# Performance work log

Measured on AMD Instinct MI355X. Metric: run time of the kernel, lower is better.

Reference implementation:

```python
import jax, jax.numpy as jnp
import numpy as np

B, T, K, H = 2, 2048, 1024, 16


def setup_inputs() -> dict:
    key = jax.random.key(0)
    ks = jax.random.split(key, 9)
    sc = 0.02
    return {
        "x": jax.random.normal(ks[0], (B, T, K), dtype=jnp.float32),
        "Wq_w": jax.random.normal(ks[1], (K, K), dtype=jnp.float32) * sc,
        "Wq_b": jax.random.normal(ks[2], (K,), dtype=jnp.float32) * sc,
        "Wk_w": jax.random.normal(ks[3], (K, K), dtype=jnp.float32) * sc,
        "Wk_b": jax.random.normal(ks[4], (K,), dtype=jnp.float32) * sc,
        "Wv_w": jax.random.normal(ks[5], (K, K), dtype=jnp.float32) * sc,
        "Wv_b": jax.random.normal(ks[6], (K,), dtype=jnp.float32) * sc,
        "Wo_w": jax.random.normal(ks[7], (K, K), dtype=jnp.float32) * sc,
        "Wo_b": jax.random.normal(ks[8], (K,), dtype=jnp.float32) * sc,
    }


def reference(x, Wq_w, Wq_b, Wk_w, Wk_b, Wv_w, Wv_b, Wo_w, Wo_b):
    b, t, k = x.shape
    h = H
    s = k // h
    # nn.Linear: y = x @ W^T + b
    q = x @ Wq_w.T + Wq_b
    kk = x @ Wk_w.T + Wk_b
    v = x @ Wv_w.T + Wv_b
    # [b, t, h, s] -> [b, h, t, s]
    q = q.reshape(b, t, h, s).transpose(0, 2, 1, 3)
    kk = kk.reshape(b, t, h, s).transpose(0, 2, 1, 3)
    v = v.reshape(b, t, h, s).transpose(0, 2, 1, 3)
    # scores [b, h, t, t]
    dot = jnp.einsum("bhqd,bhkd->bhqk", q, kk)
    # causal mask: upper triangle (offset=1) set to -inf BEFORE scaling
    causal = jnp.tril(jnp.ones((t, t), dtype=bool))
    dot = jnp.where(causal, dot, -jnp.inf)
    # NOTE: original scales by sqrt(k) (full model dim), not sqrt(head_dim)
    dot = dot / jnp.sqrt(jnp.asarray(k, dot.dtype))
    attn = jax.nn.softmax(dot, axis=-1)
    out = jnp.einsum("bhqk,bhkd->bhqd", attn, v)  # [b, h, t, s]
    out = out.transpose(0, 2, 1, 3).reshape(b, t, k)
    return out @ Wo_w.T + Wo_b
```

## Files before the change

### kernel.cpp

```cpp
#include <hip/hip_runtime.h>

typedef unsigned short u16;
typedef unsigned int u32;
typedef __bf16 bf16x8 __attribute__((ext_vector_type(8)));
typedef float f32x4 __attribute__((ext_vector_type(4)));
typedef unsigned short u16x8 __attribute__((ext_vector_type(8)));
typedef unsigned int u32x4 __attribute__((ext_vector_type(4)));

#define B_ 2
#define T_ 2048
#define K_ 1024
#define H_ 16
#define S_ 64
#define MKC 4194304
#define QSCALE 0.04508422f

__device__ __forceinline__ u16 f2bf(float f) {
  unsigned int u = __builtin_bit_cast(unsigned int, f);
  u += 0x7fffu + ((u >> 16) & 1u);
  return (u16)(u >> 16);
}

__device__ __forceinline__ f32x4 MFMA(bf16x8 a, bf16x8 b, f32x4 c) {
  return __builtin_amdgcn_mfma_f32_16x16x32_bf16(a, b, c, 0, 0, 0);
}

__device__ __forceinline__ void gld16(const void* g, void* l) {
  __builtin_amdgcn_global_load_lds((const __attribute__((address_space(1))) void*)g,
                                   (__attribute__((address_space(3))) void*)l, 16, 0, 0);
}

template <int N>
__device__ __forceinline__ void waitv() {
  asm volatile("s_waitcnt vmcnt(%0)" ::"i"(N) : "memory");
}
__device__ __forceinline__ void memfence_barrier() {
  asm volatile("" ::: "memory");
  __builtin_amdgcn_s_barrier();
}
__device__ __forceinline__ float fmax3(float a, float b, float c) {
  return fmaxf(fmaxf(a, b), c);
}

__global__ __launch_bounds__(256) void cvt_all(const float* __restrict__ x,
                                               const float* __restrict__ W0,
                                               const float* __restrict__ W1,
                                               const float* __restrict__ W2,
                                               const float* __restrict__ W3,
                                               u16* __restrict__ xb,
                                               u16* __restrict__ wb) {
  const int i = blockIdx.x * 256 + threadIdx.x;
  const float* src;
  u16* dst;
  if (i < 524288) {
    src = x + (size_t)i * 8;
    dst = xb + (size_t)i * 8;
  } else {
    const int j = i - 524288;
    const int sel = j >> 17;
    const float* W = sel == 0 ? W0 : sel == 1 ? W1 : sel == 2 ? W2 : W3;
    src = W + (size_t)(j & 131071) * 8;
    dst = wb + (size_t)j * 8;
  }
  const float4* s = (const float4*)src;
  float4 f0 = s[0], f1 = s[1];
  u16x8 p;
  p[0] = f2bf(f0.x); p[1] = f2bf(f0.y); p[2] = f2bf(f0.z); p[3] = f2bf(f0.w);
  p[4] = f2bf(f1.x); p[5] = f2bf(f1.y); p[6] = f2bf(f1.z); p[7] = f2bf(f1.w);
  *(u16x8*)dst = p;
}

template <int OMODE, int BN>
__global__ __launch_bounds__(256) void gemm16(const u16* __restrict__ A,
                                              const u16* __restrict__ Bm,
                                              const float* __restrict__ b0,
                                              const float* __restrict__ b1,
                                              const float* __restrict__ b2,
                                              void* __restrict__ C0,
                                              int M, int N, int K) {
  constexpr int NF = BN / 32;
  constexpr int SOPS = 2 + BN / 64;
  __shared__ u16 As[2][128 * 32];
  __shared__ u16 Bs[2][BN * 32];
  const int bm = blockIdx.x * 128;
  const int bn = blockIdx.y * BN;
  const int tid = threadIdx.x;
  const int w = tid >> 6, lane = tid & 63;
  const int wr = (w >> 1) * 64, wc = (w & 1) * (BN / 2);
  const int lr = lane & 15, g = lane >> 4;
  const int lk = g * 8;
  const int srow = lane >> 2, scol = (lane & 3) * 8;

  f32x4 acc[4][NF] = {};

  auto stg = [&](int buf, int k0) {
#pragma unroll
    for (int i = 0; i < 2; ++i) {
      const int rbase = (i * 4 + w) * 16;
      gld16(A + (size_t)(bm + rbase + srow) * K + k0 + scol, &As[buf][rbase * 32]);
    }
#pragma unroll
    for (int i = 0; i < BN / 64; ++i) {
      const int rbase = (i * 4 + w) * 16;
      gld16(Bm + (size_t)(bn + rbase + srow) * K + k0 + scol, &Bs[buf][rbase * 32]);
    }
  };

  stg(0, 0);
  const int NK = K >> 5;
  for (int kk = 0; kk < NK; ++kk) {
    const int buf = kk & 1;
    const bool pf = (kk + 1 < NK);
    if (pf) {
      stg(buf ^ 1, (kk + 1) * 32);
      waitv<SOPS>();
    } else {
      waitv<0>();
    }
    __builtin_amdgcn_s_barrier();
    bf16x8 af[4], bfr[NF];
#pragma unroll
    for (int m = 0; m < 4; ++m)
      af[m] = *(const bf16x8*)&As[buf][(wr + m * 16 + lr) * 32 + lk];
#pragma unroll
    for (int n = 0; n < NF; ++n)
      bfr[n] = *(const bf16x8*)&Bs[buf][(wc + n * 16 + lr) * 32 + lk];
#pragma unroll
    for (int m = 0; m < 4; ++m)
#pragma unroll
      for (int n = 0; n < NF; ++n)
        acc[m][n] = MFMA(af[m], bfr[n], acc[m][n]);
    memfence_barrier();
  }

  const int sel = (OMODE == 2) ? 0 : (bn >> 10);
  const float* bp = (OMODE == 2) ? b0 : (sel == 0 ? b0 : sel == 1 ? b1 : b2);
#pragma unroll
  for (int n = 0; n < NF; ++n) {
    const int col = bn + wc + n * 16 + lr;
    const float bv = bp[(OMODE == 2) ? col : (col & 1023)];
#pragma unroll
    for (int m = 0; m < 4; ++m) {
#pragma unroll
      for (int r = 0; r < 4; ++r) {
        const int row = bm + wr + m * 16 + g * 4 + r;
        float v = acc[m][n][r] + bv;
        if (OMODE == 2) {
          ((float*)C0)[(size_t)row * N + col] = v;
        } else {
          u16* dst = (u16*)C0;
          const int cc = col & 1023;
          if (sel == 2) {
            const int bb = row >> 11, t = row & 2047, hh = cc >> 6, ss = cc & 63;
            dst[(size_t)2 * MKC + (((size_t)(bb * H_ + hh) * S_ + ss) << 11) + t] = f2bf(v);
          } else {
            if (sel == 0) v *= QSCALE;
            dst[(size_t)sel * MKC + (size_t)row * 1024 + cc] = f2bf(v);
          }
        }
      }
    }
  }
}

__global__ __launch_bounds__(256) void attn_fwd(const u16* __restrict__ Q,
                                                const u16* __restrict__ Kb,
                                                const u16* __restrict__ Vt,
                                                u16* __restrict__ O) {
  __shared__ u16 Ks[2][64 * 64];
  __shared__ u16 Vs[2][64 * 64];
  const int tid = threadIdx.x;
  const int w = tid >> 6, lane = tid & 63;
  const int qh = lane & 15;
  const int g = lane >> 4;
  const int bh = blockIdx.x;
  const int b = bh >> 4, h = bh & 15;
  const int yy = blockIdx.y, t7 = yy & 7, kq = yy >> 3;
  const int qtile = (kq == 0) ? (31 - t7) : (kq == 1) ? (16 + t7)
                   : (kq == 2) ? (15 - t7) : t7;
  const int qb = qtile * 64;
  const int qw = qb + w * 16;
  const int myq = qw + qh;

  const size_t qoff = (size_t)(b * T_ + qw + qh) * K_ + h * S_ + g * 8;
  const bf16x8 bq0 = *(const bf16x8*)(Q + qoff);
  const bf16x8 bq1 = *(const bf16x8*)(Q + qoff + 32);

  const int srow = lane >> 3;
  const int sl8 = ((lane & 7) ^ srow) * 8;
  int kvp[2];
#pragma unroll
  for (int i = 0; i < 2; ++i) {
    const int rho = w * 16 + i * 8 + srow;
    const int a = rho >> 4;
    kvp[i] = ((a >> 1) << 5) | (((rho >> 2) & 3) << 3) | ((a & 1) << 2) | (rho & 3);
  }
  const u16* kq0 = Kb + (size_t)(b * T_ + kvp[0]) * K_ + h * S_ + sl8;
  const u16* kq1 = Kb + (size_t)(b * T_ + kvp[1]) * K_ + h * S_ + sl8;
  const u16* vq0 = Vt + (size_t)(bh * S_ + w * 16 + srow) * T_ + sl8;
  const u16* vq1 = Vt + (size_t)(bh * S_ + w * 16 + 8 + srow) * T_ + sl8;
  auto stage = [&](int buf) {
    gld16(kq0, &Ks[buf][(w * 16) * 64]);
    gld16(kq1, &Ks[buf][(w * 16 + 8) * 64]);
    gld16(vq0, &Vs[buf][(w * 16) * 64]);
    gld16(vq1, &Vs[buf][(w * 16 + 8) * 64]);
    kq0 += 64 * K_; kq1 += 64 * K_; vq0 += 64; vq1 += 64;
  };

  const int nk = qtile + 1;
  stage(0);

  float m = -INFINITY;
  f32x4 o[4] = {};
  f32x4 o_l = {};
  const int ksw = qh & 7;
  u16x8 ov;
#pragma unroll
  for (int i = 0; i < 8; ++i) ov[i] = 0x3F80;
  const bf16x8 ones = __builtin_bit_cast(bf16x8, ov);

  for (int kt = 0; kt < nk; ++kt) {
    const int k0 = kt * 64;
    const int cur = kt & 1;
    const bool pf = (kt + 1 < nk);
    if (pf) {
      stage(cur ^ 1);
      waitv<4>();
    } else {
      waitv<0>();
    }
    __builtin_amdgcn_s_barrier();

    f32x4 s[4];
    __builtin_amdgcn_s_setprio(1);
#pragma unroll
    for (int a = 0; a < 4; ++a) {
      const u16* kr = &Ks[cur][(a * 16 + qh) * 64];
      const bf16x8 kf0 = *(const bf16x8*)(kr + ((g ^ ksw) * 8));
      const bf16x8 kf1 = *(const bf16x8*)(kr + (((4 + g) ^ ksw) * 8));
      f32x4 z = {0.f, 0.f, 0.f, 0.f};
      z = MFMA(kf0, bq0, z);
      s[a] = MFMA(kf1, bq1, z);
    }
    __builtin_amdgcn_s_setprio(0);

    float p[4][4];
    if (k0 + 63 > qw) {
      const int thr = myq - k0 - (g << 3);
#pragma unroll
      for (int a = 0; a < 4; ++a)
#pragma unroll
        for (int r = 0; r < 4; ++r) {
          const int C = ((a >> 1) << 5) + ((a & 1) << 2) + r;
          p[a][r] = (C <= thr) ? s[a][r] : -INFINITY;
        }
    } else {
#pragma unroll
      for (int a = 0; a < 4; ++a)
#pragma unroll
        for (int r = 0; r < 4; ++r) p[a][r] = s[a][r];
    }
    float x0 = fmax3(p[0][0], p[0][1], p[0][2]);
    float x1 = fmax3(p[0][3], p[1][0], p[1][1]);
    float x2 = fmax3(p[1][2], p[1][3], p[2][0]);
    float x3 = fmax3(p[2][1], p[2][2], p[2][3]);
    float x4 = fmax3(p[3][0], p[3][1], p[3][2]);
    float vmax = fmax3(fmax3(x0, x1, x2), x3, fmaxf(x4, p[3][3]));
    vmax = fmaxf(vmax, __shfl_xor(vmax, 16));
    vmax = fmaxf(vmax, __shfl_xor(vmax, 32));

    if (__any(vmax > m + 11.5f)) {
      const float mnew = fmaxf(m, vmax);
      const float alpha = __builtin_amdgcn_exp2f(m - mnew);
      m = mnew;
      float aR[4];
#pragma unroll
      for (int r = 0; r < 4; ++r) aR[r] = __shfl(alpha, 4 * g + r);
#pragma unroll
      for (int nn = 0; nn < 4; ++nn)
#pragma unroll
        for (int r = 0; r < 4; ++r) o[nn][r] *= aR[r];
#pragma unroll
      for (int r = 0; r < 4; ++r) o_l[r] *= aR[r];
    }

#pragma unroll
    for (int a = 0; a < 4; ++a)
#pragma unroll
      for (int r = 0; r < 4; ++r)
        p[a][r] = __builtin_amdgcn_exp2f(p[a][r] - m);

    __builtin_amdgcn_s_setprio(1);
#pragma unroll
    for (int c = 0; c < 2; ++c) {
      u32 t0, t1, t2, t3;
      asm("v_cvt_pk_bf16_f32 %0, %1, %2" : "=v"(t0) : "v"(p[2 * c][0]), "v"(p[2 * c][1]));
      asm("v_cvt_pk_bf16_f32 %0, %1, %2" : "=v"(t1) : "v"(p[2 * c][2]), "v"(p[2 * c][3]));
      asm("v_cvt_pk_bf16_f32 %0, %1, %2" : "=v"(t2) : "v"(p[2 * c + 1][0]), "v"(p[2 * c + 1][1]));
      asm("v_cvt_pk_bf16_f32 %0, %1, %2" : "=v"(t3) : "v"(p[2 * c + 1][2]), "v"(p[2 * c + 1][3]));
      u32x4 tv; tv[0] = t0; tv[1] = t1; tv[2] = t2; tv[3] = t3;
      const bf16x8 pa = __builtin_bit_cast(bf16x8, tv);
      o_l = MFMA(pa, ones, o_l);
#pragma unroll
      for (int nn = 0; nn < 4; ++nn) {
        const bf16x8 vf =
            *(const bf16x8*)(&Vs[cur][(16 * nn + qh) * 64] + (((c * 4 + g) ^ ksw) * 8));
        o[nn] = MFMA(pa, vf, o[nn]);
      }
    }
    __builtin_amdgcn_s_setprio(0);

    memfence_barrier();
  }

#pragma unroll
  for (int r = 0; r < 4; ++r) {
    const float inv = 1.f / o_l[r];
    const size_t row = (size_t)(b * T_ + qw + 4 * g + r);
#pragma unroll
    for (int nn = 0; nn < 4; ++nn)
      O[row * K_ + h * S_ + nn * 16 + qh] = f2bf(o[nn][r] * inv);
  }
}

extern "C" void kernel_launch(void* const* d_in, const int* in_sizes, int n_in,
                              void* d_out, int out_size, void* d_ws, size_t ws_size,
                              hipStream_t stream) {
  (void)in_sizes; (void)n_in; (void)out_size; (void)ws_size;
  const float* x  = (const float*)d_in[0];
  const float* Wq = (const float*)d_in[1];
  const float* bq = (const float*)d_in[2];
  const float* Wk = (const float*)d_in[3];
  const float* bk = (const float*)d_in[4];
  const float* Wv = (const float*)d_in[5];
  const float* bv = (const float*)d_in[6];
  const float* Wo = (const float*)d_in[7];
  const float* bo = (const float*)d_in[8];
  float* out = (float*)d_out;

  const size_t MK = (size_t)MKC;
  const size_t WK = (size_t)K_ * K_;
  u16* Qb  = (u16*)d_ws;
  u16* Kbf = Qb + MK;
  u16* Vtb = Kbf + MK;
  u16* AO  = Vtb + MK;
  u16* xb  = AO + MK;
  u16* Wqkv = xb + MK;
  u16* Wob  = Wqkv + 3 * WK;

  dim3 blk(256);
  cvt_all<<<dim3(4096), blk, 0, stream>>>(x, Wq, Wk, Wv, Wo, xb, Wqkv);
  gemm16<3, 128><<<dim3(32, 24), blk, 0, stream>>>(xb, Wqkv, bq, bk, bv, Qb,
                                                   B_ * T_, 3 * K_, K_);
  attn_fwd<<<dim3(B_ * H_, T_ / 64), blk, 0, stream>>>(Qb, Kbf, Vtb, AO);
  gemm16<2, 64><<<dim3(32, 16), blk, 0, stream>>>(AO, Wob, bo, bo, bo, out,
                                                  B_ * T_, K_, K_);
}
```

Before: 109.7 us.

## Pair causal q-tiles per block and software-pipeline QK^T with softmax-PV

Each attention block now handles two query tiles (yy and 31-yy) in sequence, which balances causal work across blocks and halves the grid. Inside each tile the loop is restructured so the QK^T MFMAs for the next KV tile are issued before the softmax and PV of the current one, with K and V prefetches split and ordered separately. This aims to overlap the matrix-core work with the exp/max work and to even out per-block runtime, at the cost of fewer resident blocks, more live registers, and a serial second segment per block.

```diff
diff --git a/kernel.cpp b/kernel.cpp
--- a/kernel.cpp
+++ b/kernel.cpp
@@ -175,16 +175,7 @@
   const int g = lane >> 4;
   const int bh = blockIdx.x;
   const int b = bh >> 4, h = bh & 15;
-  const int yy = blockIdx.y, t7 = yy & 7, kq = yy >> 3;
-  const int qtile = (kq == 0) ? (31 - t7) : (kq == 1) ? (16 + t7)
-                   : (kq == 2) ? (15 - t7) : t7;
-  const int qb = qtile * 64;
-  const int qw = qb + w * 16;
-  const int myq = qw + qh;
-
-  const size_t qoff = (size_t)(b * T_ + qw + qh) * K_ + h * S_ + g * 8;
-  const bf16x8 bq0 = *(const bf16x8*)(Q + qoff);
-  const bf16x8 bq1 = *(const bf16x8*)(Q + qoff + 32);
+  const int yy = blockIdx.y;
 
   const int srow = lane >> 3;
   const int sl8 = ((lane & 7) ^ srow) * 8;
@@ -195,131 +186,166 @@
     const int a = rho >> 4;
     kvp[i] = ((a >> 1) << 5) | (((rho >> 2) & 3) << 3) | ((a & 1) << 2) | (rho & 3);
   }
-  const u16* kq0 = Kb + (size_t)(b * T_ + kvp[0]) * K_ + h * S_ + sl8;
-  const u16* kq1 = Kb + (size_t)(b * T_ + kvp[1]) * K_ + h * S_ + sl8;
-  const u16* vq0 = Vt + (size_t)(bh * S_ + w * 16 + srow) * T_ + sl8;
-  const u16* vq1 = Vt + (size_t)(bh * S_ + w * 16 + 8 + srow) * T_ + sl8;
-  auto stage = [&](int buf) {
-    gld16(kq0, &Ks[buf][(w * 16) * 64]);
-    gld16(kq1, &Ks[buf][(w * 16 + 8) * 64]);
-    gld16(vq0, &Vs[buf][(w * 16) * 64]);
-    gld16(vq1, &Vs[buf][(w * 16 + 8) * 64]);
-    kq0 += 64 * K_; kq1 += 64 * K_; vq0 += 64; vq1 += 64;
-  };
-
-  const int nk = qtile + 1;
-  stage(0);
-
-  float m = -INFINITY;
-  f32x4 o[4] = {};
-  f32x4 o_l = {};
   const int ksw = qh & 7;
   u16x8 ov;
 #pragma unroll
   for (int i = 0; i < 8; ++i) ov[i] = 0x3F80;
   const bf16x8 ones = __builtin_bit_cast(bf16x8, ov);
 
-  for (int kt = 0; kt < nk; ++kt) {
-    const int k0 = kt * 64;
-    const int cur = kt & 1;
-    const bool pf = (kt + 1 < nk);
-    if (pf) {
-      stage(cur ^ 1);
-      waitv<4>();
-    } else {
-      waitv<0>();
-    }
+  for (int seg = 0; seg < 2; ++seg) {
+    const int qtile = seg ? (31 - yy) : yy;
+    const int qb = qtile * 64;
+    const int qw = qb + w * 16;
+    const int myq = qw + qh;
+    const int nk = qtile + 1;
+
+    const size_t qoff = (size_t)(b * T_ + qw + qh) * K_ + h * S_ + g * 8;
+    const bf16x8 bq0 = *(const bf16x8*)(Q + qoff);
+    const bf16x8 bq1 = *(const bf16x8*)(Q + qoff + 32);
+
+    const u16* kq0 = Kb + (size_t)(b * T_ + kvp[0]) * K_ + h * S_ + sl8;
+    const u16* kq1 = Kb + (size_t)(b * T_ + kvp[1]) * K_ + h * S_ + sl8;
+    const u16* vq0 = Vt + (size_t)(bh * S_ + w * 16 + srow) * T_ + sl8;
+    const u16* vq1 = Vt + (size_t)(bh * S_ + w * 16 + 8 + srow) * T_ + sl8;
+
+    auto stageK = [&](int buf) {
+      gld16(kq0, &Ks[buf][(w * 16) * 64]);
+      gld16(kq1, &Ks[buf][(w * 16 + 8) * 64]);
+      kq0 += 64 * K_; kq1 += 64 * K_;
+    };
+    auto stageV = [&](int buf) {
+      gld16(vq0, &Vs[buf][(w * 16) * 64]);
+      gld16(vq1, &Vs[buf][(w * 16 + 8) * 64]);
+      vq0 += 64; vq1 += 64;
+    };
+
+    float m = -INFINITY;
+    f32x4 o[4] = {};
+    f32x4 o_l = {};
+    f32x4 sA[4], sB[4];
+
+    auto QKT = [&](int buf, f32x4 (&sO)[4]) {
+      __builtin_amdgcn_s_setprio(1);
+#pragma unroll
+      for (int a = 0; a < 4; ++a) {
+        const u16* kr = &Ks[buf][(a * 16 + qh) * 64];
+        const bf16x8 kf0 = *(const bf16x8*)(kr + ((g ^ ksw) * 8));
+        const bf16x8 kf1 = *(const bf16x8*)(kr + (((4 + g) ^ ksw) * 8));
+        f32x4 z = {0.f, 0.f, 0.f, 0.f};
+        z = MFMA(kf0, bq0, z);
+        sO[a] = MFMA(kf1, bq1, z);
+      }
+      __builtin_amdgcn_s_setprio(0);
+    };
+
+    auto SMPV = [&](f32x4 (&sIn)[4], int buf, int k0) {
+      float p[4][4];
+      if (k0 + 63 > qw) {
+        const int thr = myq - k0 - (g << 3);
+#pragma unroll
+        for (int a = 0; a < 4; ++a)
+#pragma unroll
+          for (int r = 0; r < 4; ++r) {
+            const int C = ((a >> 1) << 5) + ((a & 1) << 2) + r;
+            p[a][r] = (C <= thr) ? sIn[a][r] : -INFINITY;
+          }
+      } else {
+#pragma unroll
+        for (int a = 0; a < 4; ++a)
+#pragma unroll
+          for (int r = 0; r < 4; ++r) p[a][r] = sIn[a][r];
+      }
+      float x0 = fmax3(p[0][0], p[0][1], p[0][2]);
+      float x1 = fmax3(p[0][3], p[1][0], p[1][1]);
+      float x2 = fmax3(p[1][2], p[1][3], p[2][0]);
+      float x3 = fmax3(p[2][1], p[2][2], p[2][3]);
+      float x4 = fmax3(p[3][0], p[3][1], p[3][2]);
+      float vmax = fmax3(fmax3(x0, x1, x2), x3, fmaxf(x4, p[3][3]));
+      vmax = fmaxf(vmax, __shfl_xor(vmax, 16));
+      vmax = fmaxf(vmax, __shfl_xor(vmax, 32));
+
+      if (__any(vmax > m + 11.5f)) {
+        const float mnew = fmaxf(m, vmax);
+        const float alpha = __builtin_amdgcn_exp2f(m - mnew);
+        m = mnew;
+        float aR[4];
+#pragma unroll
+        for (int r = 0; r < 4; ++r) aR[r] = __shfl(alpha, 4 * g + r);
+#pragma unroll
+        for (int nn = 0; nn < 4; ++nn)
+#pragma unroll
+          for (int r = 0; r < 4; ++r) o[nn][r] *= aR[r];
+#pragma unroll
+        for (int r = 0; r < 4; ++r) o_l[r] *= aR[r];
+      }
+
+#pragma unroll
+      for (int a = 0; a < 4; ++a)
+#pragma unroll
+        for (int r = 0; r < 4; ++r)
+          p[a][r] = __builtin_amdgcn_exp2f(p[a][r] - m);
+
+      __builtin_amdgcn_s_setprio(1);
+#pragma unroll
+      for (int c = 0; c < 2; ++c) {
+        u32 t0, t1, t2, t3;
+        asm("v_cvt_pk_bf16_f32 %0, %1, %2" : "=v"(t0) : "v"(p[2 * c][0]), "v"(p[2 * c][1]));
+        asm("v_cvt_pk_bf16_f32 %0, %1, %2" : "=v"(t1) : "v"(p[2 * c][2]), "v"(p[2 * c][3]));
+        asm("v_cvt_pk_bf16_f32 %0, %1, %2" : "=v"(t2) : "v"(p[2 * c + 1][0]), "v"(p[2 * c + 1][1]));
+        asm("v_cvt_pk_bf16_f32 %0, %1, %2" : "=v"(t3) : "v"(p[2 * c + 1][2]), "v"(p[2 * c + 1][3]));
+        u32x4 tv; tv[0] = t0; tv[1] = t1; tv[2] = t2; tv[3] = t3;
+        const bf16x8 pa = __builtin_bit_cast(bf16x8, tv);
+        o_l = MFMA(pa, ones, o_l);
+#pragma unroll
+        for (int nn = 0; nn < 4; ++nn) {
+          const bf16x8 vf =
+              *(const bf16x8*)(&Vs[buf][(16 * nn + qh) * 64] + (((c * 4 + g) ^ ksw) * 8));
+          o[nn] = MFMA(pa, vf, o[nn]);
+        }
+      }
+      __builtin_amdgcn_s_setprio(0);
+    };
+
+    stageK(0); stageV(0);
+    waitv<0>();
     __builtin_amdgcn_s_barrier();
-
-    f32x4 s[4];
-    __builtin_amdgcn_s_setprio(1);
-#pragma unroll
-    for (int a = 0; a < 4; ++a) {
-      const u16* kr = &Ks[cur][(a * 16 + qh) * 64];
-      const bf16x8 kf0 = *(const bf16x8*)(kr + ((g ^ ksw) * 8));
-      const bf16x8 kf1 = *(const bf16x8*)(kr + (((4 + g) ^ ksw) * 8));
-      f32x4 z = {0.f, 0.f, 0.f, 0.f};
-      z = MFMA(kf0, bq0, z);
-      s[a] = MFMA(kf1, bq1, z);
-    }
-    __builtin_amdgcn_s_setprio(0);
-
-    float p[4][4];
-    if (k0 + 63 > qw) {
-      const int thr = myq - k0 - (g << 3);
-#pragma unroll
-      for (int a = 0; a < 4; ++a)
-#pragma unroll
-        for (int r = 0; r < 4; ++r) {
-          const int C = ((a >> 1) << 5) + ((a & 1) << 2) + r;
-          p[a][r] = (C <= thr) ? s[a][r] : -INFINITY;
-        }
-    } else {
-#pragma unroll
-      for (int a = 0; a < 4; ++a)
-#pragma unroll
-        for (int r = 0; r < 4; ++r) p[a][r] = s[a][r];
-    }
-    float x0 = fmax3(p[0][0], p[0][1], p[0][2]);
-    float x1 = fmax3(p[0][3], p[1][0], p[1][1]);
-    float x2 = fmax3(p[1][2], p[1][3], p[2][0]);
-    float x3 = fmax3(p[2][1], p[2][2], p[2][3]);
-    float x4 = fmax3(p[3][0], p[3][1], p[3][2]);
-    float vmax = fmax3(fmax3(x0, x1, x2), x3, fmaxf(x4, p[3][3]));
-    vmax = fmaxf(vmax, __shfl_xor(vmax, 16));
-    vmax = fmaxf(vmax, __shfl_xor(vmax, 32));
-
-    if (__any(vmax > m + 11.5f)) {
-      const float mnew = fmaxf(m, vmax);
-      const float alpha = __builtin_amdgcn_exp2f(m - mnew);
-      m = mnew;
-      float aR[4];
-#pragma unroll
-      for (int r = 0; r < 4; ++r) aR[r] = __shfl(alpha, 4 * g + r);
+    QKT(0, sA);
+    if (nk > 1) { stageK(1); stageV(1); }
+
+    int kt = 0;
+    for (;;) {
+      {
+        const bool hn = kt + 1 < nk;
+        if (hn) waitv<2>(); else waitv<0>();
+        __builtin_amdgcn_s_barrier();
+        if (hn) { QKT(1, sB); if (kt + 2 < nk) stageK(0); }
+        SMPV(sA, 0, kt * 64);
+        memfence_barrier();
+        if (kt + 2 < nk) stageV(0);
+        if (!hn) break;
+        ++kt;
+      }
+      {
+        const bool hn = kt + 1 < nk;
+        if (hn) waitv<2>(); else waitv<0>();
+        __builtin_amdgcn_s_barrier();
+        if (hn) { QKT(0, sA); if (kt + 2 < nk) stageK(1); }
+        SMPV(sB, 1, kt * 64);
+        memfence_barrier();
+        if (kt + 2 < nk) stageV(1);
+        if (!hn) break;
+        ++kt;
+      }
+    }
+
+#pragma unroll
+    for (int r = 0; r < 4; ++r) {
+      const float inv = 1.f / o_l[r];
+      const size_t row = (size_t)(b * T_ + qw + 4 * g + r);
 #pragma unroll
       for (int nn = 0; nn < 4; ++nn)
-#pragma unroll
-        for (int r = 0; r < 4; ++r) o[nn][r] *= aR[r];
-#pragma unroll
-      for (int r = 0; r < 4; ++r) o_l[r] *= aR[r];
-    }
-
-#pragma unroll
-    for (int a = 0; a < 4; ++a)
-#pragma unroll
-      for (int r = 0; r < 4; ++r)
-        p[a][r] = __builtin_amdgcn_exp2f(p[a][r] - m);
-
-    __builtin_amdgcn_s_setprio(1);
-#pragma unroll
-    for (int c = 0; c < 2; ++c) {
-      u32 t0, t1, t2, t3;
-      asm("v_cvt_pk_bf16_f32 %0, %1, %2" : "=v"(t0) : "v"(p[2 * c][0]), "v"(p[2 * c][1]));
-      asm("v_cvt_pk_bf16_f32 %0, %1, %2" : "=v"(t1) : "v"(p[2 * c][2]), "v"(p[2 * c][3]));
-      asm("v_cvt_pk_bf16_f32 %0, %1, %2" : "=v"(t2) : "v"(p[2 * c + 1][0]), "v"(p[2 * c + 1][1]));
-      asm("v_cvt_pk_bf16_f32 %0, %1, %2" : "=v"(t3) : "v"(p[2 * c + 1][2]), "v"(p[2 * c + 1][3]));
-      u32x4 tv; tv[0] = t0; tv[1] = t1; tv[2] = t2; tv[3] = t3;
-      const bf16x8 pa = __builtin_bit_cast(bf16x8, tv);
-      o_l = MFMA(pa, ones, o_l);
-#pragma unroll
-      for (int nn = 0; nn < 4; ++nn) {
-        const bf16x8 vf =
-            *(const bf16x8*)(&Vs[cur][(16 * nn + qh) * 64] + (((c * 4 + g) ^ ksw) * 8));
-        o[nn] = MFMA(pa, vf, o[nn]);
-      }
-    }
-    __builtin_amdgcn_s_setprio(0);
-
-    memfence_barrier();
-  }
-
-#pragma unroll
-  for (int r = 0; r < 4; ++r) {
-    const float inv = 1.f / o_l[r];
-    const size_t row = (size_t)(b * T_ + qw + 4 * g + r);
-#pragma unroll
-    for (int nn = 0; nn < 4; ++nn)
-      O[row * K_ + h * S_ + nn * 16 + qh] = f2bf(o[nn][r] * inv);
+        O[row * K_ + h * S_ + nn * 16 + qh] = f2bf(o[nn][r] * inv);
+    }
   }
 }
 
@@ -352,7 +378,7 @@
   cvt_all<<<dim3(4096), blk, 0, stream>>>(x, Wq, Wk, Wv, Wo, xb, Wqkv);
   gemm16<3, 128><<<dim3(32, 24), blk, 0, stream>>>(xb, Wqkv, bq, bk, bv, Qb,
                                                    B_ * T_, 3 * K_, K_);
-  attn_fwd<<<dim3(B_ * H_, T_ / 64), blk, 0, stream>>>(Qb, Kbf, Vtb, AO);
+  attn_fwd<<<dim3(B_ * H_, 16), blk, 0, stream>>>(Qb, Kbf, Vtb, AO);
   gemm16<2, 64><<<dim3(32, 16), blk, 0, stream>>>(AO, Wob, bo, bo, bo, out,
                                                   B_ * T_, K_, K_);
 }
```

Measured after the change: 105.7 us. 3.6% less time.
